# Optimization experiments

Hardware: AMD Instinct MI355X
Metric: run time of the kernel (lower is better)

## Reference

```python
import jax, jax.numpy as jnp
import numpy as np

Q_LORA = 1536
KV_LORA = 512
ROPE_DIM = 64
NOPE_DIM = 128
NUM_HEADS = 16
QK_HEAD_DIM = NOPE_DIM + ROPE_DIM  # 192
HEAD_SIZE = KV_LORA + ROPE_DIM     # 576
MAX_POS = 4096
ROPE_BASE = 10000.0
T = 32768


def _rope_cos_sin(positions):
    # inv_freq: [ROPE_DIM//2]
    inv_freq = 1.0 / (ROPE_BASE ** (jnp.arange(0, ROPE_DIM, 2, dtype=jnp.float32) / ROPE_DIM))
    freqs = positions.astype(jnp.float32)[:, None] * inv_freq[None, :]  # [T, D/2]
    return jnp.cos(freqs), jnp.sin(freqs)


def _apply_rope_neox(x, cos, sin):
    # x: [T, H, D]; cos/sin: [T, D/2] broadcast over heads
    x1, x2 = jnp.split(x, 2, axis=-1)
    c = cos[:, None, :]
    s = sin[:, None, :]
    return jnp.concatenate([x1 * c - x2 * s, x2 * c + x1 * s], axis=-1)


def setup_inputs() -> dict:
    key = jax.random.key(0)
    k1, k2, k3 = jax.random.split(key, 3)
    qkv_lora = jax.random.normal(k1, (T, Q_LORA + KV_LORA + ROPE_DIM), dtype=jnp.float32)
    positions = jax.random.randint(k2, (T,), 0, MAX_POS, dtype=jnp.int64)
    Wq = jax.random.normal(k3, (Q_LORA, NUM_HEADS * QK_HEAD_DIM), dtype=jnp.float32) * 0.02
    kv_cache = jnp.zeros((T, HEAD_SIZE), dtype=jnp.float32)
    slot_mapping = jnp.arange(T, dtype=jnp.int64)
    return {"qkv_lora": qkv_lora, "positions": positions, "Wq": Wq,
            "kv_cache": kv_cache, "slot_mapping": slot_mapping}


def reference(qkv_lora, positions, Wq, kv_cache, slot_mapping):
    # split low-rank projections
    q_c = qkv_lora[:, :Q_LORA]                               # [T, 1536]
    kv_c = qkv_lora[:, Q_LORA:Q_LORA + KV_LORA]              # [T, 512]
    k_pe = qkv_lora[:, Q_LORA + KV_LORA:]                    # [T, 64]

    # q_b_proj GEMM then reshape to heads
    q = (q_c @ Wq).reshape(T, NUM_HEADS, QK_HEAD_DIM)        # [T, H, 192]

    # RoPE on q rope slice and k_pe (neox style)
    cos, sin = _rope_cos_sin(positions)
    q_pe = _apply_rope_neox(q[..., NOPE_DIM:], cos, sin)     # [T, H, 64]
    k_pe_rot = _apply_rope_neox(k_pe[:, None, :], cos, sin)  # [T, 1, 64]
    q = jnp.concatenate([q[..., :NOPE_DIM], q_pe], axis=-1)

    # paged KV cache scatter write: concat(kv_c, k_pe) at slot_mapping
    entry = jnp.concatenate([kv_c, k_pe_rot[:, 0, :]], axis=-1)  # [T, 576]
    kv_cache = kv_cache.at[slot_mapping].set(entry)

    return q, kv_c, k_pe_rot, kv_cache
```

## Files before the change

kernel.cpp:

```cpp
#include <hip/hip_runtime.h>
#include <hip/hip_bf16.h>
#include <stdint.h>

typedef unsigned short ushort_t;
typedef __attribute__((ext_vector_type(4))) float f32x4;
typedef __attribute__((ext_vector_type(8))) short short8;

#define T_TOK 32768
#define QL    1536
#define KVL   512
#define RD    64
#define NQ    3072
#define ROWW  2112
#define HS    576

#define BM 256
#define BN 256
#define BK 64
#define KT (QL / BK)
#define MT (T_TOK / BM)
#define NT (NQ / BN)

#define ACONV_BLOCKS (T_TOK * 192 / 256)
#define WQ_BLOCKS    ((NQ / 32) * (QL / 32))
#define KVP_BLOCKS   (T_TOK / 4)

#define NLOG (-0.28782313662425572f)

static __device__ __forceinline__ short f2bf(float x) {
  __hip_bfloat16 h = __float2bfloat16(x);
  return *reinterpret_cast<short*>(&h);
}

#define GLOAD16(gp, lp)                                        \
  __builtin_amdgcn_global_load_lds(                            \
      (const __attribute__((address_space(1))) void*)(gp),     \
      (__attribute__((address_space(3))) void*)(lp), 16, 0, 0)

static __device__ __forceinline__ void kv_body(
    int tok, int lane, const float* __restrict__ qkv, const int* __restrict__ pos,
    const int* __restrict__ slots, float* __restrict__ out_kvc,
    float* __restrict__ out_kpe, float* __restrict__ out_cache) {
  const float* src = qkv + (size_t)tok * ROWW + QL;
  float* dkv = out_kvc + (size_t)tok * KVL;
  float* dc  = out_cache + (size_t)slots[tok] * HS;
#pragma unroll
  for (int i = 0; i < 2; ++i) {
    f32x4 v = *(const f32x4*)(src + (size_t)(lane + 64 * i) * 4);
    *(f32x4*)(dkv + (size_t)(lane + 64 * i) * 4) = v;
    *(f32x4*)(dc + (size_t)(lane + 64 * i) * 4) = v;
  }
  if (lane < 32) {
    float x1 = src[KVL + lane], x2 = src[KVL + 32 + lane];
    float p = (float)pos[tok];
    float invf = __expf((float)lane * NLOG);
    float s, c;
    __sincosf(p * invf, &s, &c);
    float r1 = x1 * c - x2 * s;
    float r2 = x2 * c + x1 * s;
    out_kpe[(size_t)tok * RD + lane] = r1;
    out_kpe[(size_t)tok * RD + 32 + lane] = r2;
    dc[KVL + lane] = r1;
    dc[KVL + 32 + lane] = r2;
  }
}

__global__ __launch_bounds__(256) void pre_kernel(
    const float* __restrict__ qkv, ushort_t* __restrict__ Abf,
    const float* __restrict__ Wq, ushort_t* __restrict__ Wt,
    const int* __restrict__ pos, const int* __restrict__ slots,
    float* __restrict__ out_kvc, float* __restrict__ out_kpe,
    float* __restrict__ out_cache, int do_kv) {
  __shared__ float tile[32][33];
  int bid = blockIdx.x, tid = threadIdx.x;
  if (bid < ACONV_BLOCKS) {
    int g = bid * 256 + tid;
    int row = g / 192;
    int col = (g - row * 192) * 8;
    const float* s = qkv + (size_t)row * ROWW + col;
    f32x4 a = *(const f32x4*)s;
    f32x4 b = *(const f32x4*)(s + 4);
    short8 v;
    v[0] = f2bf(a[0]); v[1] = f2bf(a[1]); v[2] = f2bf(a[2]); v[3] = f2bf(a[3]);
    v[4] = f2bf(b[0]); v[5] = f2bf(b[1]); v[6] = f2bf(b[2]); v[7] = f2bf(b[3]);
    *(short8*)(Abf + (size_t)row * QL + col) = v;
  } else if (bid < ACONV_BLOCKS + WQ_BLOCKS) {
    int b2 = bid - ACONV_BLOCKS;
    int n0 = (b2 % (NQ / 32)) * 32, k0 = (b2 / (NQ / 32)) * 32;
    int tx = tid & 31, ty = tid >> 5;
#pragma unroll
    for (int j = 0; j < 32; j += 8)
      tile[ty + j][tx] = Wq[(size_t)(k0 + ty + j) * NQ + n0 + tx];
    __syncthreads();
#pragma unroll
    for (int j = 0; j < 32; j += 8)
      Wt[(size_t)(n0 + ty + j) * QL + k0 + tx] = f2bf(tile[tx][ty + j]);
  } else if (do_kv) {
    int b3 = bid - ACONV_BLOCKS - WQ_BLOCKS;
    int tok = b3 * 4 + (tid >> 6);
    kv_body(tok, tid & 63, qkv, pos, slots, out_kvc, out_kpe, out_cache);
  }
}

__global__ __launch_bounds__(512, 2) void gemm_rope_kernel(
    const ushort_t* __restrict__ Abf, const int* __restrict__ pos,
    const ushort_t* __restrict__ wt, float* __restrict__ out_q) {
  __shared__ ushort_t lds[2][2][2][256 * 32];

  int bid = blockIdx.x;
  int vb = (bid & 7) * (MT * NT / 8) + (bid >> 3);
  int m0 = (vb / NT) * BM;
  int n0 = (vb % NT) * BN;

  int tid = threadIdx.x;
  int wv = tid >> 6, ln = tid & 63;
  int l16 = ln & 15, lq4 = ln >> 4;
  int wm = wv >> 2, wn = wv & 3;

  int srow = wv * 32 + (ln >> 2);
  int schunk = ((ln & 3) ^ ((ln >> 3) & 3)) * 8;
  const ushort_t* aS = Abf + (size_t)(m0 + srow) * QL + schunk;
  const ushort_t* bS = wt  + (size_t)(n0 + srow) * QL + schunk;
  int sdst = wv * 32 * 32;

#define STG(PAR, AB, KH, TT, SRC) do {                                         \
    GLOAD16((SRC) + (size_t)(TT) * BK + (KH) * 32,           &lds[PAR][AB][KH][sdst]);       \
    GLOAD16((SRC) + (size_t)(TT) * BK + (KH) * 32 + 16 * QL, &lds[PAR][AB][KH][sdst + 512]); \
  } while (0)

  int rkey = (l16 >> 1) & 3;
  int aoff = (wm * 128 + l16) * 32 + (lq4 ^ rkey) * 8;
  int boff = (wn * 64  + l16) * 32 + (lq4 ^ rkey) * 8;

  f32x4 acc[8][4];
#pragma unroll
  for (int i = 0; i < 8; ++i)
#pragma unroll
    for (int j = 0; j < 4; ++j) acc[i][j] = (f32x4)0.0f;

  STG(0, 0, 0, 0, aS);
  STG(0, 1, 0, 0, bS);
  STG(0, 0, 1, 0, aS);
  STG(0, 1, 1, 0, bS);
  STG(1, 0, 0, 1, aS);
  STG(1, 1, 0, 1, bS);

#define CLUSTER(ACCBASE, AF, BF)                                               \
  __builtin_amdgcn_s_setprio(1);                                               \
  _Pragma("unroll")                                                            \
  for (int q = 0; q < 4; ++q)                                                  \
    _Pragma("unroll")                                                          \
    for (int n = 0; n < 4; ++n)                                                \
      acc[(ACCBASE) + q][n] = __builtin_amdgcn_mfma_f32_16x16x32_bf16(         \
          AF[q], BF[n], acc[(ACCBASE) + q][n], 0, 0, 0);                       \
  __builtin_amdgcn_s_setprio(0);

#pragma unroll 2
  for (int t = 0; t < KT; ++t) {
    int par = t & 1;
    const ushort_t* Ak0 = &lds[par][0][0][0];
    const ushort_t* Bk0 = &lds[par][1][0][0];
    const ushort_t* Ak1 = &lds[par][0][1][0];
    const ushort_t* Bk1 = &lds[par][1][1][0];
    short8 af0[4], af1[4], bf0[4], ag0[4], ag1[4], bg0[4];

    __builtin_amdgcn_sched_barrier(0);
    if (t == KT - 1) { asm volatile("s_waitcnt vmcnt(0)" ::: "memory"); }
    else             { asm volatile("s_waitcnt vmcnt(4)" ::: "memory"); }
    __builtin_amdgcn_s_barrier();
    __builtin_amdgcn_sched_barrier(0);

#pragma unroll
    for (int q = 0; q < 4; ++q) af0[q] = *(const short8*)(Ak0 + aoff + q * 512);
#pragma unroll
    for (int n = 0; n < 4; ++n) bf0[n] = *(const short8*)(Bk0 + boff + n * 512);
#pragma unroll
    for (int q = 0; q < 4; ++q) af1[q] = *(const short8*)(Ak0 + aoff + (4 + q) * 512);
    if (t + 1 < KT) { STG(par ^ 1, 0, 1, t + 1, aS); STG(par ^ 1, 1, 1, t + 1, bS); }

    CLUSTER(0, af0, bf0)
    CLUSTER(4, af1, bf0)

#pragma unroll
    for (int q = 0; q < 4; ++q) ag0[q] = *(const short8*)(Ak1 + aoff + q * 512);
#pragma unroll
    for (int n = 0; n < 4; ++n) bg0[n] = *(const short8*)(Bk1 + boff + n * 512);
#pragma unroll
    for (int q = 0; q < 4; ++q) ag1[q] = *(const short8*)(Ak1 + aoff + (4 + q) * 512);

    __builtin_amdgcn_sched_barrier(0);
    __builtin_amdgcn_s_barrier();
    __builtin_amdgcn_sched_barrier(0);
    if (t + 2 < KT) { STG(par, 0, 0, t + 2, aS); STG(par, 1, 0, t + 2, bS); }

    CLUSTER(0, ag0, bg0)
    CLUSTER(4, ag1, bg0)
  }

  int gn = n0 + wn * 64;
  bool ropew = ((gn % 192) == 128);
  if (!ropew) {
#pragma unroll
    for (int mi = 0; mi < 8; ++mi)
#pragma unroll
      for (int r = 0; r < 4; ++r) {
        int t = m0 + wm * 128 + mi * 16 + lq4 * 4 + r;
        float* rowp = out_q + (size_t)t * NQ + gn + l16;
        rowp[0]  = acc[mi][0][r];
        rowp[16] = acc[mi][1][r];
        rowp[32] = acc[mi][2][r];
        rowp[48] = acc[mi][3][r];
      }
  } else {
    float invf0 = __expf((float)l16 * NLOG);
    float invf1 = __expf((float)(l16 + 16) * NLOG);
#pragma unroll
    for (int mi = 0; mi < 8; ++mi)
#pragma unroll
      for (int r = 0; r < 4; ++r) {
        int t = m0 + wm * 128 + mi * 16 + lq4 * 4 + r;
        float p = (float)pos[t];
        float s0, c0, s1, c1;
        __sincosf(p * invf0, &s0, &c0);
        __sincosf(p * invf1, &s1, &c1);
        float x1a = acc[mi][0][r], x1b = acc[mi][1][r];
        float x2a = acc[mi][2][r], x2b = acc[mi][3][r];
        float* rowp = out_q + (size_t)t * NQ + gn + l16;
        rowp[0]  = x1a * c0 - x2a * s0;
        rowp[16] = x1b * c1 - x2b * s1;
        rowp[32] = x2a * c0 + x1a * s0;
        rowp[48] = x2b * c1 + x1b * s1;
      }
  }
}

__global__ void kv_kernel(const float* __restrict__ qkv, const int* __restrict__ pos,
                          const int* __restrict__ slots,
                          float* __restrict__ out_kvc, float* __restrict__ out_kpe,
                          float* __restrict__ out_cache) {
  int tok = blockIdx.x * 4 + (threadIdx.x >> 6);
  kv_body(tok, threadIdx.x & 63, qkv, pos, slots, out_kvc, out_kpe, out_cache);
}

extern "C" void kernel_launch(void* const* d_in, const int* in_sizes, int n_in,
                              void* d_out, int out_size, void* d_ws, size_t ws_size,
                              hipStream_t stream) {
  const float* qkv       = (const float*)d_in[0];
  const int*   positions = (const int*)d_in[1];
  const float* Wq        = (const float*)d_in[2];
  const int*   slots     = (const int*)d_in[4];

  float* out_q     = (float*)d_out;
  float* out_kvc   = out_q   + (size_t)T_TOK * NQ;
  float* out_kpe   = out_kvc + (size_t)T_TOK * KVL;
  float* out_cache = out_kpe + (size_t)T_TOK * RD;

  size_t abf_bytes = (size_t)T_TOK * QL * sizeof(ushort_t);
  size_t wt_bytes  = (size_t)NQ * QL * sizeof(ushort_t);
  int ws_ok = (ws_size >= abf_bytes + wt_bytes);
  char* scratch = ws_ok ? (char*)d_ws : (char*)out_kvc;
  ushort_t* Abf = (ushort_t*)scratch;
  ushort_t* Wt  = (ushort_t*)(scratch + abf_bytes);

  int pre_blocks = ACONV_BLOCKS + WQ_BLOCKS + (ws_ok ? KVP_BLOCKS : 0);
  pre_kernel<<<dim3(pre_blocks), dim3(256), 0, stream>>>(
      qkv, Abf, Wq, Wt, positions, slots, out_kvc, out_kpe, out_cache, ws_ok);
  gemm_rope_kernel<<<dim3(MT * NT), dim3(512), 0, stream>>>(Abf, positions, Wt, out_q);
  if (!ws_ok)
    kv_kernel<<<dim3(KVP_BLOCKS), dim3(256), 0, stream>>>(qkv, positions, slots,
                                                          out_kvc, out_kpe, out_cache);
}
```

Measured before the change: 431.9 us.

## Restructure GEMM main loop with one sync per K-tile and staggered wave MFMA

Result: slower. 451.4 us (+4.5%).

```diff
diff --git a/kernel.cpp b/kernel.cpp
--- a/kernel.cpp
+++ b/kernel.cpp
@@ -116,6 +116,7 @@
   int wv = tid >> 6, ln = tid & 63;
   int l16 = ln & 15, lq4 = ln >> 4;
   int wm = wv >> 2, wn = wv & 3;
+  const bool g1 = (wm != 0);
 
   int srow = wv * 32 + (ln >> 2);
   int schunk = ((ln & 3) ^ ((ln >> 3) & 3)) * 8;
@@ -138,12 +139,13 @@
 #pragma unroll
     for (int j = 0; j < 4; ++j) acc[i][j] = (f32x4)0.0f;
 
+  short8 af0[4], af1[4], bf0[4];
+  short8 ag0[4], ag1[4], bg[4];
+
   STG(0, 0, 0, 0, aS);
   STG(0, 1, 0, 0, bS);
   STG(0, 0, 1, 0, aS);
   STG(0, 1, 1, 0, bS);
-  STG(1, 0, 0, 1, aS);
-  STG(1, 1, 0, 1, bS);
 
 #define CLUSTER(ACCBASE, AF, BF)                                               \
   __builtin_amdgcn_s_setprio(1);                                               \
@@ -162,40 +164,38 @@
     const ushort_t* Bk0 = &lds[par][1][0][0];
     const ushort_t* Ak1 = &lds[par][0][1][0];
     const ushort_t* Bk1 = &lds[par][1][1][0];
-    short8 af0[4], af1[4], bf0[4], ag0[4], ag1[4], bg0[4];
-
-    __builtin_amdgcn_sched_barrier(0);
-    if (t == KT - 1) { asm volatile("s_waitcnt vmcnt(0)" ::: "memory"); }
-    else             { asm volatile("s_waitcnt vmcnt(4)" ::: "memory"); }
-    __builtin_amdgcn_s_barrier();
-    __builtin_amdgcn_sched_barrier(0);
+
+    __syncthreads();
+
+    if (g1 && t > 0) { CLUSTER(4, ag1, bg) }
 
 #pragma unroll
     for (int q = 0; q < 4; ++q) af0[q] = *(const short8*)(Ak0 + aoff + q * 512);
 #pragma unroll
     for (int n = 0; n < 4; ++n) bf0[n] = *(const short8*)(Bk0 + boff + n * 512);
+
+    if (t + 1 < KT) {
+      STG(par ^ 1, 0, 0, t + 1, aS);
+      STG(par ^ 1, 1, 0, t + 1, bS);
+      STG(par ^ 1, 0, 1, t + 1, aS);
+      STG(par ^ 1, 1, 1, t + 1, bS);
+    }
+
+    CLUSTER(0, af0, bf0)
 #pragma unroll
     for (int q = 0; q < 4; ++q) af1[q] = *(const short8*)(Ak0 + aoff + (4 + q) * 512);
-    if (t + 1 < KT) { STG(par ^ 1, 0, 1, t + 1, aS); STG(par ^ 1, 1, 1, t + 1, bS); }
-
-    CLUSTER(0, af0, bf0)
     CLUSTER(4, af1, bf0)
 
 #pragma unroll
     for (int q = 0; q < 4; ++q) ag0[q] = *(const short8*)(Ak1 + aoff + q * 512);
 #pragma unroll
-    for (int n = 0; n < 4; ++n) bg0[n] = *(const short8*)(Bk1 + boff + n * 512);
+    for (int n = 0; n < 4; ++n) bg[n]  = *(const short8*)(Bk1 + boff + n * 512);
+    CLUSTER(0, ag0, bg)
 #pragma unroll
     for (int q = 0; q < 4; ++q) ag1[q] = *(const short8*)(Ak1 + aoff + (4 + q) * 512);
-
-    __builtin_amdgcn_sched_barrier(0);
-    __builtin_amdgcn_s_barrier();
-    __builtin_amdgcn_sched_barrier(0);
-    if (t + 2 < KT) { STG(par, 0, 0, t + 2, aS); STG(par, 1, 0, t + 2, bS); }
-
-    CLUSTER(0, ag0, bg0)
-    CLUSTER(4, ag1, bg0)
-  }
+    if (!g1) { CLUSTER(4, ag1, bg) }
+  }
+  if (g1) { CLUSTER(4, ag1, bg) }
 
   int gn = n0 + wn * 64;
   bool ropew = ((gn % 192) == 128);
```

## Load GEMM B fragments directly from global memory, bypassing LDS staging

Applied to the files above, without the earlier changes.

Measured after the change: 634.2 us. 1.47x slower.

```diff
diff --git a/kernel.cpp b/kernel.cpp
--- a/kernel.cpp
+++ b/kernel.cpp
@@ -105,12 +105,12 @@
 __global__ __launch_bounds__(512, 2) void gemm_rope_kernel(
     const ushort_t* __restrict__ Abf, const int* __restrict__ pos,
     const ushort_t* __restrict__ wt, float* __restrict__ out_q) {
-  __shared__ ushort_t lds[2][2][2][256 * 32];
+  __shared__ ushort_t lds[2][2][256 * 32];
 
   int bid = blockIdx.x;
   int vb = (bid & 7) * (MT * NT / 8) + (bid >> 3);
-  int m0 = (vb / NT) * BM;
-  int n0 = (vb % NT) * BN;
+  int m0 = (vb % MT) * BM;
+  int n0 = (vb / MT) * BN;
 
   int tid = threadIdx.x;
   int wv = tid >> 6, ln = tid & 63;
@@ -120,17 +120,17 @@
   int srow = wv * 32 + (ln >> 2);
   int schunk = ((ln & 3) ^ ((ln >> 3) & 3)) * 8;
   const ushort_t* aS = Abf + (size_t)(m0 + srow) * QL + schunk;
-  const ushort_t* bS = wt  + (size_t)(n0 + srow) * QL + schunk;
   int sdst = wv * 32 * 32;
 
-#define STG(PAR, AB, KH, TT, SRC) do {                                         \
-    GLOAD16((SRC) + (size_t)(TT) * BK + (KH) * 32,           &lds[PAR][AB][KH][sdst]);       \
-    GLOAD16((SRC) + (size_t)(TT) * BK + (KH) * 32 + 16 * QL, &lds[PAR][AB][KH][sdst + 512]); \
+#define STG(PAR, KH, TT) do {                                                  \
+    GLOAD16(aS + (size_t)(TT) * BK + (KH) * 32,           &lds[PAR][KH][sdst]);       \
+    GLOAD16(aS + (size_t)(TT) * BK + (KH) * 32 + 16 * QL, &lds[PAR][KH][sdst + 512]); \
   } while (0)
 
   int rkey = (l16 >> 1) & 3;
   int aoff = (wm * 128 + l16) * 32 + (lq4 ^ rkey) * 8;
-  int boff = (wn * 64  + l16) * 32 + (lq4 ^ rkey) * 8;
+
+  const ushort_t* bGf = wt + (size_t)(n0 + wn * 64 + l16) * QL + lq4 * 8;
 
   f32x4 acc[8][4];
 #pragma unroll
@@ -138,12 +138,9 @@
 #pragma unroll
     for (int j = 0; j < 4; ++j) acc[i][j] = (f32x4)0.0f;
 
-  STG(0, 0, 0, 0, aS);
-  STG(0, 1, 0, 0, bS);
-  STG(0, 0, 1, 0, aS);
-  STG(0, 1, 1, 0, bS);
-  STG(1, 0, 0, 1, aS);
-  STG(1, 1, 0, 1, bS);
+  STG(0, 0, 0);
+  STG(0, 1, 0);
+  STG(1, 0, 1);
 
 #define CLUSTER(ACCBASE, AF, BF)                                               \
   __builtin_amdgcn_s_setprio(1);                                               \
@@ -158,43 +155,43 @@
 #pragma unroll 2
   for (int t = 0; t < KT; ++t) {
     int par = t & 1;
-    const ushort_t* Ak0 = &lds[par][0][0][0];
-    const ushort_t* Bk0 = &lds[par][1][0][0];
-    const ushort_t* Ak1 = &lds[par][0][1][0];
-    const ushort_t* Bk1 = &lds[par][1][1][0];
-    short8 af0[4], af1[4], bf0[4], ag0[4], ag1[4], bg0[4];
+    const ushort_t* Ak0 = &lds[par][0][0];
+    const ushort_t* Ak1 = &lds[par][1][0];
+    short8 af0[4], af1[4], ag0[4], ag1[4], bc0[4], bc1[4];
 
     __builtin_amdgcn_sched_barrier(0);
     if (t == KT - 1) { asm volatile("s_waitcnt vmcnt(0)" ::: "memory"); }
-    else             { asm volatile("s_waitcnt vmcnt(4)" ::: "memory"); }
+    else             { asm volatile("s_waitcnt vmcnt(2)" ::: "memory"); }
     __builtin_amdgcn_s_barrier();
     __builtin_amdgcn_sched_barrier(0);
 
 #pragma unroll
+    for (int n = 0; n < 4; ++n) {
+      bc0[n] = *(const short8*)(bGf + (size_t)n * 16 * QL + t * BK);
+      bc1[n] = *(const short8*)(bGf + (size_t)n * 16 * QL + t * BK + 32);
+    }
+
+#pragma unroll
     for (int q = 0; q < 4; ++q) af0[q] = *(const short8*)(Ak0 + aoff + q * 512);
-#pragma unroll
-    for (int n = 0; n < 4; ++n) bf0[n] = *(const short8*)(Bk0 + boff + n * 512);
+    if (t + 1 < KT) STG(par ^ 1, 1, t + 1);
+
+    CLUSTER(0, af0, bc0)
 #pragma unroll
     for (int q = 0; q < 4; ++q) af1[q] = *(const short8*)(Ak0 + aoff + (4 + q) * 512);
-    if (t + 1 < KT) { STG(par ^ 1, 0, 1, t + 1, aS); STG(par ^ 1, 1, 1, t + 1, bS); }
-
-    CLUSTER(0, af0, bf0)
-    CLUSTER(4, af1, bf0)
+    CLUSTER(4, af1, bc0)
 
 #pragma unroll
     for (int q = 0; q < 4; ++q) ag0[q] = *(const short8*)(Ak1 + aoff + q * 512);
 #pragma unroll
-    for (int n = 0; n < 4; ++n) bg0[n] = *(const short8*)(Bk1 + boff + n * 512);
-#pragma unroll
     for (int q = 0; q < 4; ++q) ag1[q] = *(const short8*)(Ak1 + aoff + (4 + q) * 512);
 
     __builtin_amdgcn_sched_barrier(0);
     __builtin_amdgcn_s_barrier();
     __builtin_amdgcn_sched_barrier(0);
-    if (t + 2 < KT) { STG(par, 0, 0, t + 2, aS); STG(par, 1, 0, t + 2, bS); }
-
-    CLUSTER(0, ag0, bg0)
-    CLUSTER(4, ag1, bg0)
+    if (t + 2 < KT) STG(par, 0, t + 2);
+
+    CLUSTER(0, ag0, bc1)
+    CLUSTER(4, ag1, bc1)
   }
 
   int gn = n0 + wn * 64;
```
